# Kernel optimization log

Measured on AMD Instinct MI355X. Metric: run time of the kernel, lower is better.

Reference implementation:

```python
import jax, jax.numpy as jnp
import numpy as np

B, S, D = 2, 2048, 2048      # batch, seq, hidden_dim
F = 4096                      # expert ffn dim
E, K = 8, 2                   # num_experts, top_k


def setup_inputs() -> dict:
    key = jax.random.key(0)
    k0, k1, k2, k3, k4 = jax.random.split(key, 5)
    sc_d = 1.0 / np.sqrt(D)
    sc_f = 1.0 / np.sqrt(F)
    return {
        "hidden_states": jax.random.normal(k0, (B, S, D), jnp.float32),
        "gate_w": jax.random.normal(k1, (E, D), jnp.float32) * sc_d,  # router Linear(D->E)
        "w1": jax.random.normal(k2, (E, F, D), jnp.float32) * sc_d,   # stacked expert w1
        "w2": jax.random.normal(k3, (E, D, F), jnp.float32) * sc_f,   # stacked expert w2
        "w3": jax.random.normal(k4, (E, F, D), jnp.float32) * sc_d,   # stacked expert w3
    }


def reference(hidden_states, gate_w, w1, w2, w3):
    b, s, d = hidden_states.shape
    x = hidden_states.reshape(-1, d)                    # [T, D]
    T = x.shape[0]

    # Router: softmax in float32, top-k, renormalize (matches torch code)
    logits = x @ gate_w.T                               # [T, E]
    probs = jax.nn.softmax(logits.astype(jnp.float32), axis=-1)
    top_w, top_e = jax.lax.top_k(probs, K)              # [T, K]
    top_w = top_w / jnp.sum(top_w, axis=-1, keepdims=True)
    top_w = top_w.astype(x.dtype)

    # Scatter top-k weights into dense per-expert weight matrix [T, E]
    rows = jnp.arange(T)[:, None]
    w_full = jnp.zeros((T, E), x.dtype).at[rows, top_e].set(top_w)

    # Expert SwiGLU MLPs; dense-per-expert with zero weight for unrouted tokens
    # is mathematically identical to the gather/scatter loop in the original.
    y = jnp.zeros_like(x)
    for e in range(E):
        h = jax.nn.silu(x @ w1[e].T) * (x @ w3[e].T)    # [T, F]
        y = y + w_full[:, e:e + 1] * (h @ w2[e].T)      # [T, D]

    return y.reshape(b, s, d)
```

## Files before the change

### kernel.cpp

```cpp
#include <hip/hip_runtime.h>
#include <hip/hip_bf16.h>

#define TTOK 4096
#define DIM  2048
#define FF   4096
#define NE   8
#define TROWS 8192

#define BM 256
#define BK 64

typedef __attribute__((ext_vector_type(4))) float  f32x4;
typedef __attribute__((ext_vector_type(8))) short  s16x8;
typedef __attribute__((ext_vector_type(8))) unsigned short u16x8;

__device__ __forceinline__ unsigned short f2bf(float f) {
  union { __hip_bfloat16 h; unsigned short u; } cv;
  cv.h = __float2bfloat16(f);
  return cv.u;
}
__device__ __forceinline__ float bf2f(unsigned short u) {
  union { unsigned int i; float f; } cv;
  cv.i = ((unsigned int)u) << 16;
  return cv.f;
}

__device__ __forceinline__ void gl_lds16(const void* g, void* s) {
  __builtin_amdgcn_global_load_lds(
      (__attribute__((address_space(1))) void*)(g),
      (__attribute__((address_space(3))) void*)(s), 16, 0, 0);
}

#define VMW(NN) asm volatile("s_waitcnt vmcnt(" #NN ")" ::: "memory")

#define MIDSYNC do { \
    __builtin_amdgcn_sched_barrier(0); \
    __builtin_amdgcn_s_barrier(); \
    asm volatile("s_waitcnt lgkmcnt(0)" ::: "memory"); \
    __builtin_amdgcn_sched_barrier(0); \
  } while (0)
#define ENDB do { \
    __builtin_amdgcn_sched_barrier(0); \
    __builtin_amdgcn_s_barrier(); \
  } while (0)

__global__ __launch_bounds__(256) void cvt_kernel(const float* __restrict__ s,
                                                  unsigned short* __restrict__ d, int n8) {
  int i = blockIdx.x * 256 + threadIdx.x;
  if (i >= n8) return;
  f32x4 v0 = *(const f32x4*)(s + (size_t)i * 8);
  f32x4 v1 = *(const f32x4*)(s + (size_t)i * 8 + 4);
  u16x8 o;
#pragma unroll
  for (int j = 0; j < 4; ++j) { o[j] = f2bf(v0[j]); o[j + 4] = f2bf(v1[j]); }
  *(u16x8*)(d + (size_t)i * 8) = o;
}

__global__ void router_kernel(const float* __restrict__ x,
                              const float* __restrict__ gate_w,
                              int* __restrict__ tope, float* __restrict__ topw,
                              int* __restrict__ counts) {
  const int t = blockIdx.x;
  const int tid = threadIdx.x;
  const float* xr = x + (size_t)t * DIM;
  float p[NE];
#pragma unroll
  for (int e = 0; e < NE; ++e) p[e] = 0.f;
  for (int d = tid; d < DIM; d += 256) {
    float xv = xr[d];
#pragma unroll
    for (int e = 0; e < NE; ++e) p[e] += xv * gate_w[e * DIM + d];
  }
#pragma unroll
  for (int off = 32; off > 0; off >>= 1) {
#pragma unroll
    for (int e = 0; e < NE; ++e) p[e] += __shfl_down(p[e], off);
  }
  __shared__ float red[4][NE];
  const int wid = tid >> 6, lane = tid & 63;
  if (lane == 0) {
#pragma unroll
    for (int e = 0; e < NE; ++e) red[wid][e] = p[e];
  }
  __syncthreads();
  if (tid == 0) {
    float l[NE];
#pragma unroll
    for (int e = 0; e < NE; ++e) l[e] = red[0][e] + red[1][e] + red[2][e] + red[3][e];
    float mx = l[0];
#pragma unroll
    for (int e = 1; e < NE; ++e) mx = fmaxf(mx, l[e]);
    float pr[NE]; float sum = 0.f;
#pragma unroll
    for (int e = 0; e < NE; ++e) { pr[e] = __expf(l[e] - mx); sum += pr[e]; }
    float inv = 1.f / sum;
#pragma unroll
    for (int e = 0; e < NE; ++e) pr[e] *= inv;
    int i0 = 0; float p0 = pr[0];
#pragma unroll
    for (int e = 1; e < NE; ++e) if (pr[e] > p0) { p0 = pr[e]; i0 = e; }
    int i1 = -1; float p1 = -1.f;
#pragma unroll
    for (int e = 0; e < NE; ++e) if (e != i0 && pr[e] > p1) { p1 = pr[e]; i1 = e; }
    float wsum = p0 + p1;
    tope[t * 2 + 0] = i0; topw[t * 2 + 0] = p0 / wsum;
    tope[t * 2 + 1] = i1; topw[t * 2 + 1] = p1 / wsum;
    atomicAdd(&counts[i0], 1);
    atomicAdd(&counts[i1], 1);
  }
}

__global__ void prefix_kernel(const int* __restrict__ counts, int* __restrict__ basep) {
  if (threadIdx.x == 0 && blockIdx.x == 0) {
    int acc = 0;
    for (int e = 0; e < NE; ++e) { basep[e] = acc; acc += counts[e]; }
  }
}

__global__ void fill_kernel(const int* __restrict__ tope, const float* __restrict__ topw,
                            const int* __restrict__ basep, int* __restrict__ fillp,
                            int* __restrict__ rowtok, float* __restrict__ roww,
                            int* __restrict__ rowof) {
  int t = blockIdx.x * blockDim.x + threadIdx.x;
  if (t >= TTOK) return;
#pragma unroll
  for (int s = 0; s < 2; ++s) {
    int e = tope[t * 2 + s];
    int r = basep[e] + atomicAdd(&fillp[e], 1);
    rowtok[r] = t;
    roww[r] = topw[t * 2 + s];
    rowof[t * 2 + s] = r;
  }
}

__global__ __launch_bounds__(512, 1) void gemm1f(
    const unsigned short* __restrict__ xb, const unsigned short* __restrict__ w1b,
    const unsigned short* __restrict__ w3b, const int* __restrict__ rowtok,
    const int* __restrict__ counts, const int* __restrict__ basep,
    unsigned short* __restrict__ H) {
  constexpr int GX = FF / 128;
  constexpr int GY = TTOK / BM;
  constexpr int Q  = GX * GY;
  int lin = (blockIdx.z * GY + blockIdx.y) * GX + blockIdx.x;
  int wg = (lin & 7) * Q + (lin >> 3);
  const int e   = wg / (GX * GY);
  const int rem = wg % (GX * GY);
  const int m0  = (rem / GX) * BM;
  const int n0  = (rem % GX) * 128;

  const int cnt = counts[e];
  if (m0 >= cnt) return;
  const int base_e = basep[e];

  __shared__ unsigned short As[2][BM * BK];
  __shared__ unsigned short B1s[2][128 * BK];
  __shared__ unsigned short B3s[2][128 * BK];

  const int tid = threadIdx.x;
  const int lane = tid & 63;
  const int w = tid >> 6;
  const int wm = w >> 2;
  const int wn = w & 3;

  const int lsub  = lane >> 3;
  const int lslot = lane & 7;
  const int swz_e = 8 * (lslot ^ lsub);

  const unsigned short* pA[4];
  const unsigned short* pB1[2];
  const unsigned short* pB3[2];
#pragma unroll
  for (int s = 0; s < 4; ++s) {
    int rl = s * 64 + w * 8 + lsub;
    int ga = m0 + rl; if (ga > cnt - 1) ga = cnt - 1;
    int tok = rowtok[base_e + ga];
    pA[s] = xb + (size_t)tok * DIM + swz_e;
  }
#pragma unroll
  for (int s = 0; s < 2; ++s) {
    int rl = s * 64 + w * 8 + lsub;
    pB1[s] = w1b + ((size_t)e * FF + n0 + rl) * DIM + swz_e;
    pB3[s] = w3b + ((size_t)e * FF + n0 + rl) * DIM + swz_e;
  }

  const int frow = lane & 15;
  const int klane = lane >> 4;
  const int ks0 = (klane * 8) ^ ((frow & 7) * 8);
  const int ks1 = (32 + klane * 8) ^ ((frow & 7) * 8);

  f32x4 acc1[8][2], acc3[8][2];
#pragma unroll
  for (int mf = 0; mf < 8; ++mf)
#pragma unroll
    for (int nf = 0; nf < 2; ++nf) { acc1[mf][nf] = (f32x4)0.f; acc3[mf][nf] = (f32x4)0.f; }

#define ST_A(BUF, G0, T) do { \
    gl_lds16(pA[G0]     + (size_t)(T) * BK, &As[BUF][((G0) * 64 + w * 8) * BK]); \
    gl_lds16(pA[(G0)+1] + (size_t)(T) * BK, &As[BUF][(((G0)+1) * 64 + w * 8) * BK]); \
  } while (0)
#define ST_B1(BUF, T) do { \
    gl_lds16(pB1[0] + (size_t)(T) * BK, &B1s[BUF][(0  + w * 8) * BK]); \
    gl_lds16(pB1[1] + (size_t)(T) * BK, &B1s[BUF][(64 + w * 8) * BK]); \
  } while (0)
#define ST_B3(BUF, T) do { \
    gl_lds16(pB3[0] + (size_t)(T) * BK, &B3s[BUF][(0  + w * 8) * BK]); \
    gl_lds16(pB3[1] + (size_t)(T) * BK, &B3s[BUF][(64 + w * 8) * BK]); \
  } while (0)

#define RD_A(MH, BUF) do { \
    _Pragma("unroll") \
    for (int ii = 0; ii < 4; ++ii) { \
      a[ii][0] = *(const s16x8*)&As[BUF][(wm * 128 + (MH) * 64 + ii * 16 + frow) * BK + ks0]; \
      a[ii][1] = *(const s16x8*)&As[BUF][(wm * 128 + (MH) * 64 + ii * 16 + frow) * BK + ks1]; \
    } } while (0)
#define RD_BX(DST, ARR, BUF) do { \
    _Pragma("unroll") \
    for (int j = 0; j < 2; ++j) { \
      DST[j][0] = *(const s16x8*)&ARR[BUF][(wn * 32 + j * 16 + frow) * BK + ks0]; \
      DST[j][1] = *(const s16x8*)&ARR[BUF][(wn * 32 + j * 16 + frow) * BK + ks1]; \
    } } while (0)

#define MMX(ACC, MH, BB) do { \
    __builtin_amdgcn_s_setprio(1); \
    _Pragma("unroll") \
    for (int ii = 0; ii < 4; ++ii) \
      _Pragma("unroll") \
      for (int j = 0; j < 2; ++j) { \
        ACC[(MH) * 4 + ii][j] = __builtin_amdgcn_mfma_f32_16x16x32_bf16( \
            a[ii][0], BB[j][0], ACC[(MH) * 4 + ii][j], 0, 0, 0); \
        ACC[(MH) * 4 + ii][j] = __builtin_amdgcn_mfma_f32_16x16x32_bf16( \
            a[ii][1], BB[j][1], ACC[(MH) * 4 + ii][j], 0, 0, 0); \
      } \
    __builtin_amdgcn_s_setprio(0); \
  } while (0)

  const int NT = DIM / BK;

  ST_A(0, 0, 0); ST_A(0, 2, 0);
  ST_B1(0, 0); ST_B3(0, 0);
  ST_B1(1, 1); ST_B3(1, 1);
  ST_A(1, 0, 1); ST_A(1, 2, 1);
  VMW(8);
  __builtin_amdgcn_s_barrier();

  s16x8 a[4][2], bl[2][2], bh[2][2];

  for (int t = 0; t < NT; t += 2) {
    const bool full = (t + 2 < NT);

    RD_A(0, 0); RD_BX(bl, B1s, 0);
    MIDSYNC; MMX(acc1, 0, bl); ENDB;
    RD_BX(bh, B3s, 0);
    if (full) ST_B1(0, t + 2);
    MIDSYNC; MMX(acc3, 0, bh); ENDB;
    RD_A(1, 0);
    if (full) ST_B3(0, t + 2);
    MIDSYNC; MMX(acc3, 1, bh); ENDB;
    if (full) { ST_A(0, 0, t + 2); ST_A(0, 2, t + 2); }
    MIDSYNC; MMX(acc1, 1, bl);
    if (full) { VMW(8); } else { VMW(0); }
    ENDB;

    RD_A(0, 1); RD_BX(bl, B1s, 1);
    MIDSYNC; MMX(acc1, 0, bl); ENDB;
    RD_BX(bh, B3s, 1);
    if (full) ST_B1(1, t + 3);
    MIDSYNC; MMX(acc3, 0, bh); ENDB;
    RD_A(1, 1);
    if (full) ST_B3(1, t + 3);
    MIDSYNC; MMX(acc3, 1, bh); ENDB;
    if (full) { ST_A(1, 0, t + 3); ST_A(1, 2, t + 3); }
    MIDSYNC; MMX(acc1, 1, bl);
    if (full) { VMW(8); }
    ENDB;
  }
#undef ST_A
#undef ST_B1
#undef ST_B3
#undef RD_A
#undef RD_BX
#undef MMX

#pragma unroll
  for (int mf = 0; mf < 8; ++mf) {
#pragma unroll
    for (int nf = 0; nf < 2; ++nf) {
      int col = n0 + wn * 32 + nf * 16 + frow;
      f32x4 c1 = acc1[mf][nf], c3 = acc3[mf][nf];
#pragma unroll
      for (int j = 0; j < 4; ++j) {
        int rl = wm * 128 + (mf >> 2) * 64 + (mf & 3) * 16 + klane * 4 + j;
        int grow = m0 + rl;
        if (grow < cnt) {
          float s = c1[j];
          float hval = (s / (1.f + __expf(-s))) * c3[j];
          H[(size_t)(base_e + grow) * FF + col] = f2bf(hval);
        }
      }
    }
  }
}

template <int K, int N>
__global__ __launch_bounds__(512, 1) void gemm8(
    const unsigned short* __restrict__ Asrc, const unsigned short* __restrict__ Bw,
    const float* __restrict__ roww, const int* __restrict__ counts,
    const int* __restrict__ basep, float* __restrict__ Out) {
  constexpr int GX = N / BM;
  constexpr int GY = TTOK / BM;
  constexpr int Q  = GX * GY;
  int lin = (blockIdx.z * GY + blockIdx.y) * GX + blockIdx.x;
  int wg = (lin & 7) * Q + (lin >> 3);
  const int e   = wg / (GX * GY);
  const int rem = wg % (GX * GY);
  const int m0  = (rem / GX) * BM;
  const int n0  = (rem % GX) * BM;

  const int cnt = counts[e];
  if (m0 >= cnt) return;
  const int base_e = basep[e];

  __shared__ unsigned short As[2][BM * BK];
  __shared__ unsigned short Bs[2][BM * BK];

  const int tid = threadIdx.x;
  const int lane = tid & 63;
  const int w = tid >> 6;
  const int wm = w >> 2;
  const int wn = w & 3;

  const int lsub  = lane >> 3;
  const int lslot = lane & 7;
  const int swz_e = 8 * (lslot ^ lsub);

  const unsigned short* pA[4];
  const unsigned short* pB[4];
#pragma unroll
  for (int s = 0; s < 4; ++s) {
    int rl = s * 64 + w * 8 + lsub;
    int ga = m0 + rl; if (ga > cnt - 1) ga = cnt - 1;
    pA[s] = Asrc + (size_t)(base_e + ga) * K + swz_e;
    pB[s] = Bw + ((size_t)e * N + n0 + rl) * K + swz_e;
  }

  const int frow = lane & 15;
  const int klane = lane >> 4;
  const int ks0 = (klane * 8) ^ ((frow & 7) * 8);
  const int ks1 = (32 + klane * 8) ^ ((frow & 7) * 8);

  f32x4 acc[8][4];
#pragma unroll
  for (int mf = 0; mf < 8; ++mf)
#pragma unroll
    for (int nf = 0; nf < 4; ++nf) acc[mf][nf] = (f32x4)0.f;

#define ST_A(BUF, G0, T) do { \
    gl_lds16(pA[G0]     + (size_t)(T) * BK, &As[BUF][((G0) * 64 + w * 8) * BK]); \
    gl_lds16(pA[(G0)+1] + (size_t)(T) * BK, &As[BUF][(((G0)+1) * 64 + w * 8) * BK]); \
  } while (0)
#define ST_B(BUF, G0, T) do { \
    gl_lds16(pB[G0]     + (size_t)(T) * BK, &Bs[BUF][((G0) * 64 + w * 8) * BK]); \
    gl_lds16(pB[(G0)+1] + (size_t)(T) * BK, &Bs[BUF][(((G0)+1) * 64 + w * 8) * BK]); \
  } while (0)

#define RD_A(MH, BUF) do { \
    _Pragma("unroll") \
    for (int ii = 0; ii < 4; ++ii) { \
      a[ii][0] = *(const s16x8*)&As[BUF][(wm * 128 + (MH) * 64 + ii * 16 + frow) * BK + ks0]; \
      a[ii][1] = *(const s16x8*)&As[BUF][(wm * 128 + (MH) * 64 + ii * 16 + frow) * BK + ks1]; \
    } } while (0)
#define RD_B(DST, NH, BUF) do { \
    _Pragma("unroll") \
    for (int j = 0; j < 2; ++j) { \
      DST[j][0] = *(const s16x8*)&Bs[BUF][(wn * 64 + (NH) * 32 + j * 16 + frow) * BK + ks0]; \
      DST[j][1] = *(const s16x8*)&Bs[BUF][(wn * 64 + (NH) * 32 + j * 16 + frow) * BK + ks1]; \
    } } while (0)

#define MM(MH, NH, BB) do { \
    __builtin_amdgcn_s_setprio(1); \
    _Pragma("unroll") \
    for (int ii = 0; ii < 4; ++ii) \
      _Pragma("unroll") \
      for (int j = 0; j < 2; ++j) { \
        acc[(MH) * 4 + ii][(NH) * 2 + j] = __builtin_amdgcn_mfma_f32_16x16x32_bf16( \
            a[ii][0], BB[j][0], acc[(MH) * 4 + ii][(NH) * 2 + j], 0, 0, 0); \
        acc[(MH) * 4 + ii][(NH) * 2 + j] = __builtin_amdgcn_mfma_f32_16x16x32_bf16( \
            a[ii][1], BB[j][1], acc[(MH) * 4 + ii][(NH) * 2 + j], 0, 0, 0); \
      } \
    __builtin_amdgcn_s_setprio(0); \
  } while (0)

  const int NT = K / BK;

  ST_A(0, 0, 0); ST_A(0, 2, 0);
  ST_B(0, 0, 0); ST_B(0, 2, 0);
  ST_B(1, 0, 1); ST_B(1, 2, 1);
  ST_A(1, 0, 1); ST_A(1, 2, 1);
  VMW(8);
  __builtin_amdgcn_s_barrier();

  s16x8 a[4][2], bl[2][2], bh[2][2];

  for (int t = 0; t < NT; t += 2) {
    const bool full = (t + 2 < NT);

    RD_A(0, 0); RD_B(bl, 0, 0);
    MIDSYNC; MM(0, 0, bl); ENDB;
    RD_B(bh, 1, 0);
    MIDSYNC; MM(0, 1, bh); ENDB;
    RD_A(1, 0);
    if (full) ST_B(0, 0, t + 2);
    MIDSYNC; MM(1, 1, bh); ENDB;
    if (full) { ST_B(0, 2, t + 2); ST_A(0, 0, t + 2); ST_A(0, 2, t + 2); }
    MIDSYNC; MM(1, 0, bl);
    if (full) { VMW(8); } else { VMW(0); }
    ENDB;

    RD_A(0, 1); RD_B(bl, 0, 1);
    MIDSYNC; MM(0, 0, bl); ENDB;
    RD_B(bh, 1, 1);
    MIDSYNC; MM(0, 1, bh); ENDB;
    RD_A(1, 1);
    if (full) ST_B(1, 0, t + 3);
    MIDSYNC; MM(1, 1, bh); ENDB;
    if (full) { ST_B(1, 2, t + 3); ST_A(1, 0, t + 3); ST_A(1, 2, t + 3); }
    MIDSYNC; MM(1, 0, bl);
    if (full) { VMW(8); }
    ENDB;
  }
#undef ST_A
#undef ST_B
#undef RD_A
#undef RD_B
#undef MM

#pragma unroll
  for (int mf = 0; mf < 8; ++mf) {
#pragma unroll
    for (int nf = 0; nf < 4; ++nf) {
      int col = n0 + wn * 64 + nf * 16 + frow;
#pragma unroll
      for (int j = 0; j < 4; ++j) {
        int rl = wm * 128 + (mf >> 2) * 64 + (mf & 3) * 16 + klane * 4 + j;
        int grow = m0 + rl;
        if (grow < cnt) {
          float wv = roww[base_e + grow];
          Out[(size_t)(base_e + grow) * N + col] = acc[mf][nf][j] * wv;
        }
      }
    }
  }
}

__global__ __launch_bounds__(256) void combine_kernel(const float* __restrict__ R,
                                                      const int* __restrict__ rowof,
                                                      float* __restrict__ y) {
  int idx = blockIdx.x * 256 + threadIdx.x;
  int t = idx >> 9;
  int d4 = idx & 511;
  int r0 = rowof[t * 2], r1 = rowof[t * 2 + 1];
  f32x4 a = *(const f32x4*)(R + (size_t)r0 * DIM + d4 * 4);
  f32x4 b = *(const f32x4*)(R + (size_t)r1 * DIM + d4 * 4);
  *(f32x4*)(y + (size_t)t * DIM + d4 * 4) = a + b;
}

extern "C" void kernel_launch(void* const* d_in, const int* in_sizes, int n_in,
                              void* d_out, int out_size, void* d_ws, size_t ws_size,
                              hipStream_t stream) {
  const float* x      = (const float*)d_in[0];
  const float* gate_w = (const float*)d_in[1];
  const float* w1     = (const float*)d_in[2];
  const float* w2     = (const float*)d_in[3];
  const float* w3     = (const float*)d_in[4];
  float* y = (float*)d_out;

  char* ws = (char*)d_ws;
  const size_t MB = 1ull << 20;
  int*   tope   = (int*)(ws);
  float* topw   = (float*)(ws + (32 << 10));
  int*   rowtok = (int*)(ws + (64 << 10));
  float* roww   = (float*)(ws + (96 << 10));
  int*   rowof  = (int*)(ws + (128 << 10));
  int*   counts = (int*)(ws + (160 << 10));
  int*   basep  = counts + 32;
  int*   fillp  = counts + 64;

  unsigned short* xb  = (unsigned short*)(ws + 1 * MB);
  unsigned short* H1  = (unsigned short*)(ws + 17 * MB);
  unsigned short* w1b = (unsigned short*)(ws + 145 * MB);
  unsigned short* w3b = (unsigned short*)(ws + 273 * MB);
  unsigned short* w2b = (unsigned short*)(ws + 401 * MB);
  float*          R   = (float*)(ws + 81 * MB);

  hipMemsetAsync(counts, 0, 512, stream);
  router_kernel<<<TTOK, 256, 0, stream>>>(x, gate_w, tope, topw, counts);
  prefix_kernel<<<1, 64, 0, stream>>>(counts, basep);
  fill_kernel<<<TTOK / 256, 256, 0, stream>>>(tope, topw, basep, fillp, rowtok, roww, rowof);

  const int nw8 = NE * FF * DIM / 8;
  const int nx8 = TTOK * DIM / 8;
  cvt_kernel<<<nw8 / 256, 256, 0, stream>>>(w1, w1b, nw8);
  cvt_kernel<<<nw8 / 256, 256, 0, stream>>>(w3, w3b, nw8);
  cvt_kernel<<<nw8 / 256, 256, 0, stream>>>(w2, w2b, nw8);
  cvt_kernel<<<nx8 / 256, 256, 0, stream>>>(x, xb, nx8);

  gemm1f<<<dim3(FF / 128, TTOK / BM, NE), 512, 0, stream>>>(
      xb, w1b, w3b, rowtok, counts, basep, H1);
  gemm8<FF, DIM><<<dim3(DIM / BM, TTOK / BM, NE), 512, 0, stream>>>(
      H1, w2b, roww, counts, basep, R);
  combine_kernel<<<TTOK * DIM / 4 / 256, 256, 0, stream>>>(R, rowof, y);
}
```

Measured before the change: 1.008 ms.

## Fuse fp32-to-bf16 weight conversion into the expert GEMM B-tile loads

The separate conversion kernels for w1, w3 and w2 are removed. Each GEMM now loads fp32 weight tiles into registers, converts them to bf16, and writes them into swizzled LDS inside its software pipeline, replacing the direct global-to-LDS copies. This avoids writing and re-reading roughly 400MB of bf16 weight copies per call. In exchange, every M-tile re-reads fp32 weights at twice the bytes, and the kernels carry extra registers and VALU conversion work. The tile order also changes so that M varies fastest within an expert, to improve weight reuse in L2.

```diff
diff --git a/kernel.cpp b/kernel.cpp
--- a/kernel.cpp
+++ b/kernel.cpp
@@ -134,8 +134,8 @@
 }
 
 __global__ __launch_bounds__(512, 1) void gemm1f(
-    const unsigned short* __restrict__ xb, const unsigned short* __restrict__ w1b,
-    const unsigned short* __restrict__ w3b, const int* __restrict__ rowtok,
+    const unsigned short* __restrict__ xb, const float* __restrict__ w1,
+    const float* __restrict__ w3, const int* __restrict__ rowtok,
     const int* __restrict__ counts, const int* __restrict__ basep,
     unsigned short* __restrict__ H) {
   constexpr int GX = FF / 128;
@@ -143,10 +143,10 @@
   constexpr int Q  = GX * GY;
   int lin = (blockIdx.z * GY + blockIdx.y) * GX + blockIdx.x;
   int wg = (lin & 7) * Q + (lin >> 3);
-  const int e   = wg / (GX * GY);
-  const int rem = wg % (GX * GY);
-  const int m0  = (rem / GX) * BM;
-  const int n0  = (rem % GX) * 128;
+  const int e   = wg / Q;
+  const int rem = wg % Q;
+  const int m0  = (rem % GY) * BM;
+  const int n0  = (rem / GY) * 128;
 
   const int cnt = counts[e];
   if (m0 >= cnt) return;
@@ -167,8 +167,6 @@
   const int swz_e = 8 * (lslot ^ lsub);
 
   const unsigned short* pA[4];
-  const unsigned short* pB1[2];
-  const unsigned short* pB3[2];
 #pragma unroll
   for (int s = 0; s < 4; ++s) {
     int rl = s * 64 + w * 8 + lsub;
@@ -176,11 +174,13 @@
     int tok = rowtok[base_e + ga];
     pA[s] = xb + (size_t)tok * DIM + swz_e;
   }
-#pragma unroll
-  for (int s = 0; s < 2; ++s) {
-    int rl = s * 64 + w * 8 + lsub;
-    pB1[s] = w1b + ((size_t)e * FF + n0 + rl) * DIM + swz_e;
-    pB3[s] = w3b + ((size_t)e * FF + n0 + rl) * DIM + swz_e;
+  const float* qB1[2];
+  const float* qB3[2];
+#pragma unroll
+  for (int g = 0; g < 2; ++g) {
+    int rl = n0 + g * 64 + w * 8 + lsub;
+    qB1[g] = w1 + ((size_t)e * FF + rl) * DIM + lslot * 8;
+    qB3[g] = w3 + ((size_t)e * FF + rl) * DIM + lslot * 8;
   }
 
   const int frow = lane & 15;
@@ -198,14 +198,22 @@
     gl_lds16(pA[G0]     + (size_t)(T) * BK, &As[BUF][((G0) * 64 + w * 8) * BK]); \
     gl_lds16(pA[(G0)+1] + (size_t)(T) * BK, &As[BUF][(((G0)+1) * 64 + w * 8) * BK]); \
   } while (0)
-#define ST_B1(BUF, T) do { \
-    gl_lds16(pB1[0] + (size_t)(T) * BK, &B1s[BUF][(0  + w * 8) * BK]); \
-    gl_lds16(pB1[1] + (size_t)(T) * BK, &B1s[BUF][(64 + w * 8) * BK]); \
-  } while (0)
-#define ST_B3(BUF, T) do { \
-    gl_lds16(pB3[0] + (size_t)(T) * BK, &B3s[BUF][(0  + w * 8) * BK]); \
-    gl_lds16(pB3[1] + (size_t)(T) * BK, &B3s[BUF][(64 + w * 8) * BK]); \
-  } while (0)
+
+#define LD_BQ(RB, Q, T) do { \
+    _Pragma("unroll") \
+    for (int g = 0; g < 2; ++g) { \
+      RB[g * 2]     = *(const f32x4*)(Q[g] + (size_t)(T) * BK); \
+      RB[g * 2 + 1] = *(const f32x4*)(Q[g] + (size_t)(T) * BK + 4); \
+    } } while (0)
+#define WR_BX(RB, ARR, BUF) do { \
+    _Pragma("unroll") \
+    for (int g = 0; g < 2; ++g) { \
+      u16x8 o; \
+      _Pragma("unroll") \
+      for (int j = 0; j < 4; ++j) { \
+        o[j] = f2bf(RB[g * 2][j]); o[j + 4] = f2bf(RB[g * 2 + 1][j]); } \
+      *(u16x8*)&ARR[BUF][(g * 64 + w * 8 + lsub) * BK + swz_e] = o; \
+    } } while (0)
 
 #define RD_A(MH, BUF) do { \
     _Pragma("unroll") \
@@ -236,47 +244,51 @@
 
   const int NT = DIM / BK;
 
-  ST_A(0, 0, 0); ST_A(0, 2, 0);
-  ST_B1(0, 0); ST_B3(0, 0);
-  ST_B1(1, 1); ST_B3(1, 1);
-  ST_A(1, 0, 1); ST_A(1, 2, 1);
-  VMW(8);
-  __builtin_amdgcn_s_barrier();
+  {
+    ST_A(0, 0, 0); ST_A(0, 2, 0);
+    ST_A(1, 0, 1); ST_A(1, 2, 1);
+    f32x4 r10[4], r30[4], r11[4], r31[4];
+    LD_BQ(r10, qB1, 0); LD_BQ(r30, qB3, 0);
+    LD_BQ(r11, qB1, 1); LD_BQ(r31, qB3, 1);
+    WR_BX(r10, B1s, 0); WR_BX(r30, B3s, 0);
+    WR_BX(r11, B1s, 1); WR_BX(r31, B3s, 1);
+    asm volatile("s_waitcnt lgkmcnt(0)" ::: "memory");
+    VMW(0);
+    __builtin_amdgcn_s_barrier();
+  }
 
   s16x8 a[4][2], bl[2][2], bh[2][2];
+  f32x4 rb1[4], rb3[4];
 
   for (int t = 0; t < NT; t += 2) {
     const bool full = (t + 2 < NT);
 
     RD_A(0, 0); RD_BX(bl, B1s, 0);
+    if (full) { LD_BQ(rb1, qB1, t + 2); LD_BQ(rb3, qB3, t + 2); }
     MIDSYNC; MMX(acc1, 0, bl); ENDB;
     RD_BX(bh, B3s, 0);
-    if (full) ST_B1(0, t + 2);
     MIDSYNC; MMX(acc3, 0, bh); ENDB;
     RD_A(1, 0);
-    if (full) ST_B3(0, t + 2);
+    if (full) WR_BX(rb1, B1s, 0);
     MIDSYNC; MMX(acc3, 1, bh); ENDB;
-    if (full) { ST_A(0, 0, t + 2); ST_A(0, 2, t + 2); }
-    MIDSYNC; MMX(acc1, 1, bl);
-    if (full) { VMW(8); } else { VMW(0); }
-    ENDB;
+    if (full) { WR_BX(rb3, B3s, 0); ST_A(0, 0, t + 2); ST_A(0, 2, t + 2); }
+    else VMW(0);
+    MIDSYNC; MMX(acc1, 1, bl); ENDB;
 
     RD_A(0, 1); RD_BX(bl, B1s, 1);
+    if (full) { LD_BQ(rb1, qB1, t + 3); LD_BQ(rb3, qB3, t + 3); }
     MIDSYNC; MMX(acc1, 0, bl); ENDB;
     RD_BX(bh, B3s, 1);
-    if (full) ST_B1(1, t + 3);
     MIDSYNC; MMX(acc3, 0, bh); ENDB;
     RD_A(1, 1);
-    if (full) ST_B3(1, t + 3);
+    if (full) WR_BX(rb1, B1s, 1);
     MIDSYNC; MMX(acc3, 1, bh); ENDB;
-    if (full) { ST_A(1, 0, t + 3); ST_A(1, 2, t + 3); }
-    MIDSYNC; MMX(acc1, 1, bl);
-    if (full) { VMW(8); }
-    ENDB;
+    if (full) { WR_BX(rb3, B3s, 1); ST_A(1, 0, t + 3); ST_A(1, 2, t + 3); }
+    MIDSYNC; MMX(acc1, 1, bl); ENDB;
   }
 #undef ST_A
-#undef ST_B1
-#undef ST_B3
+#undef LD_BQ
+#undef WR_BX
 #undef RD_A
 #undef RD_BX
 #undef MMX
@@ -303,7 +315,7 @@
 
 template <int K, int N>
 __global__ __launch_bounds__(512, 1) void gemm8(
-    const unsigned short* __restrict__ Asrc, const unsigned short* __restrict__ Bw,
+    const unsigned short* __restrict__ Asrc, const float* __restrict__ Bw,
     const float* __restrict__ roww, const int* __restrict__ counts,
     const int* __restrict__ basep, float* __restrict__ Out) {
   constexpr int GX = N / BM;
@@ -311,10 +323,10 @@
   constexpr int Q  = GX * GY;
   int lin = (blockIdx.z * GY + blockIdx.y) * GX + blockIdx.x;
   int wg = (lin & 7) * Q + (lin >> 3);
-  const int e   = wg / (GX * GY);
-  const int rem = wg % (GX * GY);
-  const int m0  = (rem / GX) * BM;
-  const int n0  = (rem % GX) * BM;
+  const int e   = wg / Q;
+  const int rem = wg % Q;
+  const int m0  = (rem % GY) * BM;
+  const int n0  = (rem / GY) * BM;
 
   const int cnt = counts[e];
   if (m0 >= cnt) return;
@@ -334,13 +346,13 @@
   const int swz_e = 8 * (lslot ^ lsub);
 
   const unsigned short* pA[4];
-  const unsigned short* pB[4];
+  const float* qB[4];
 #pragma unroll
   for (int s = 0; s < 4; ++s) {
     int rl = s * 64 + w * 8 + lsub;
     int ga = m0 + rl; if (ga > cnt - 1) ga = cnt - 1;
     pA[s] = Asrc + (size_t)(base_e + ga) * K + swz_e;
-    pB[s] = Bw + ((size_t)e * N + n0 + rl) * K + swz_e;
+    qB[s] = Bw + ((size_t)e * N + n0 + rl) * K + lslot * 8;
   }
 
   const int frow = lane & 15;
@@ -358,10 +370,21 @@
     gl_lds16(pA[G0]     + (size_t)(T) * BK, &As[BUF][((G0) * 64 + w * 8) * BK]); \
     gl_lds16(pA[(G0)+1] + (size_t)(T) * BK, &As[BUF][(((G0)+1) * 64 + w * 8) * BK]); \
   } while (0)
-#define ST_B(BUF, G0, T) do { \
-    gl_lds16(pB[G0]     + (size_t)(T) * BK, &Bs[BUF][((G0) * 64 + w * 8) * BK]); \
-    gl_lds16(pB[(G0)+1] + (size_t)(T) * BK, &Bs[BUF][(((G0)+1) * 64 + w * 8) * BK]); \
-  } while (0)
+#define LD_BG(RB, S0, T) do { \
+    _Pragma("unroll") \
+    for (int gg = 0; gg < 2; ++gg) { \
+      RB[gg * 2]     = *(const f32x4*)(qB[(S0) + gg] + (size_t)(T) * BK); \
+      RB[gg * 2 + 1] = *(const f32x4*)(qB[(S0) + gg] + (size_t)(T) * BK + 4); \
+    } } while (0)
+#define WR_BG(RB, S0, BUF) do { \
+    _Pragma("unroll") \
+    for (int gg = 0; gg < 2; ++gg) { \
+      u16x8 o; \
+      _Pragma("unroll") \
+      for (int j = 0; j < 4; ++j) { \
+        o[j] = f2bf(RB[gg * 2][j]); o[j + 4] = f2bf(RB[gg * 2 + 1][j]); } \
+      *(u16x8*)&Bs[BUF][(((S0) + gg) * 64 + w * 8 + lsub) * BK + swz_e] = o; \
+    } } while (0)
 
 #define RD_A(MH, BUF) do { \
     _Pragma("unroll") \
@@ -392,44 +415,53 @@
 
   const int NT = K / BK;
 
-  ST_A(0, 0, 0); ST_A(0, 2, 0);
-  ST_B(0, 0, 0); ST_B(0, 2, 0);
-  ST_B(1, 0, 1); ST_B(1, 2, 1);
-  ST_A(1, 0, 1); ST_A(1, 2, 1);
-  VMW(8);
-  __builtin_amdgcn_s_barrier();
+  {
+    ST_A(0, 0, 0); ST_A(0, 2, 0);
+    ST_A(1, 0, 1); ST_A(1, 2, 1);
+    f32x4 rl0[4], rh0[4], rl1[4], rh1[4];
+    LD_BG(rl0, 0, 0); LD_BG(rh0, 2, 0);
+    LD_BG(rl1, 0, 1); LD_BG(rh1, 2, 1);
+    WR_BG(rl0, 0, 0); WR_BG(rh0, 2, 0);
+    WR_BG(rl1, 0, 1); WR_BG(rh1, 2, 1);
+    asm volatile("s_waitcnt lgkmcnt(0)" ::: "memory");
+    VMW(0);
+    __builtin_amdgcn_s_barrier();
+  }
 
   s16x8 a[4][2], bl[2][2], bh[2][2];
+  f32x4 rbl[4], rbh[4];
 
   for (int t = 0; t < NT; t += 2) {
     const bool full = (t + 2 < NT);
 
     RD_A(0, 0); RD_B(bl, 0, 0);
+    if (full) LD_BG(rbl, 0, t + 2);
     MIDSYNC; MM(0, 0, bl); ENDB;
     RD_B(bh, 1, 0);
+    if (full) LD_BG(rbh, 2, t + 2);
     MIDSYNC; MM(0, 1, bh); ENDB;
     RD_A(1, 0);
-    if (full) ST_B(0, 0, t + 2);
+    if (full) WR_BG(rbl, 0, 0);
     MIDSYNC; MM(1, 1, bh); ENDB;
-    if (full) { ST_B(0, 2, t + 2); ST_A(0, 0, t + 2); ST_A(0, 2, t + 2); }
-    MIDSYNC; MM(1, 0, bl);
-    if (full) { VMW(8); } else { VMW(0); }
-    ENDB;
+    if (full) { WR_BG(rbh, 2, 0); ST_A(0, 0, t + 2); ST_A(0, 2, t + 2); }
+    else VMW(0);
+    MIDSYNC; MM(1, 0, bl); ENDB;
 
     RD_A(0, 1); RD_B(bl, 0, 1);
+    if (full) LD_BG(rbl, 0, t + 3);
     MIDSYNC; MM(0, 0, bl); ENDB;
     RD_B(bh, 1, 1);
+    if (full) LD_BG(rbh, 2, t + 3);
     MIDSYNC; MM(0, 1, bh); ENDB;
     RD_A(1, 1);
-    if (full) ST_B(1, 0, t + 3);
+    if (full) WR_BG(rbl, 0, 1);
     MIDSYNC; MM(1, 1, bh); ENDB;
-    if (full) { ST_B(1, 2, t + 3); ST_A(1, 0, t + 3); ST_A(1, 2, t + 3); }
-    MIDSYNC; MM(1, 0, bl);
-    if (full) { VMW(8); }
-    ENDB;
+    if (full) { WR_BG(rbh, 2, 1); ST_A(1, 0, t + 3); ST_A(1, 2, t + 3); }
+    MIDSYNC; MM(1, 0, bl); ENDB;
   }
 #undef ST_A
-#undef ST_B
+#undef LD_BG
+#undef WR_BG
 #undef RD_A
 #undef RD_B
 #undef MM
@@ -485,28 +517,21 @@
   int*   basep  = counts + 32;
   int*   fillp  = counts + 64;
 
-  unsigned short* xb  = (unsigned short*)(ws + 1 * MB);
-  unsigned short* H1  = (unsigned short*)(ws + 17 * MB);
-  unsigned short* w1b = (unsigned short*)(ws + 145 * MB);
-  unsigned short* w3b = (unsigned short*)(ws + 273 * MB);
-  unsigned short* w2b = (unsigned short*)(ws + 401 * MB);
-  float*          R   = (float*)(ws + 81 * MB);
+  unsigned short* xb = (unsigned short*)(ws + 1 * MB);
+  unsigned short* H1 = (unsigned short*)(ws + 17 * MB);
+  float*          R  = (float*)(ws + 81 * MB);
 
   hipMemsetAsync(counts, 0, 512, stream);
   router_kernel<<<TTOK, 256, 0, stream>>>(x, gate_w, tope, topw, counts);
   prefix_kernel<<<1, 64, 0, stream>>>(counts, basep);
   fill_kernel<<<TTOK / 256, 256, 0, stream>>>(tope, topw, basep, fillp, rowtok, roww, rowof);
 
-  const int nw8 = NE * FF * DIM / 8;
   const int nx8 = TTOK * DIM / 8;
-  cvt_kernel<<<nw8 / 256, 256, 0, stream>>>(w1, w1b, nw8);
-  cvt_kernel<<<nw8 / 256, 256, 0, stream>>>(w3, w3b, nw8);
-  cvt_kernel<<<nw8 / 256, 256, 0, stream>>>(w2, w2b, nw8);
   cvt_kernel<<<nx8 / 256, 256, 0, stream>>>(x, xb, nx8);
 
   gemm1f<<<dim3(FF / 128, TTOK / BM, NE), 512, 0, stream>>>(
-      xb, w1b, w3b, rowtok, counts, basep, H1);
+      xb, w1, w3, rowtok, counts, basep, H1);
   gemm8<FF, DIM><<<dim3(DIM / BM, TTOK / BM, NE), 512, 0, stream>>>(
-      H1, w2b, roww, counts, basep, R);
+      H1, w2, roww, counts, basep, R);
   combine_kernel<<<TTOK * DIM / 4 / 256, 256, 0, stream>>>(R, rowof, y);
 }
```

Measured after the change: 2.095 ms. 2.08x slower.
